# Kernel optimization log

Measured on AMD Instinct MI355X. Metric: run time of the kernel, lower is better.

The kernel has to match this reference:

```python
import jax, jax.numpy as jnp
import numpy as np

NH = 8          # attention heads
NC = 14         # disease classes
K = 10          # aspect queries per class
E = 1024        # vision_dim == text_dim
HID = 512       # hidden_dim = vision_dim // 2
TEMP = 0.1
LN_EPS = 1e-5


def _layernorm(x, g, b):
    m = jnp.mean(x, axis=-1, keepdims=True)
    v = jnp.mean(jnp.square(x - m), axis=-1, keepdims=True)
    return (x - m) * jax.lax.rsqrt(v + LN_EPS) * g + b


def _mha(q, k, v, in_w, in_b, out_w, out_b):
    # nn.MultiheadAttention (batch_first, eval mode => dropout off)
    B, Lq, Emb = q.shape
    Lk = k.shape[1]
    dh = Emb // NH
    wq, wk, wv = jnp.split(in_w, 3, axis=0)
    bq, bk, bv = jnp.split(in_b, 3)
    qh = (q @ wq.T + bq).reshape(B, Lq, NH, dh)
    kh = (k @ wk.T + bk).reshape(B, Lk, NH, dh)
    vh = (v @ wv.T + bv).reshape(B, Lk, NH, dh)
    scale = np.float32(1.0 / np.sqrt(dh))
    scores = jnp.einsum('bqhd,bkhd->bhqk', qh, kh) * scale
    attn = jax.nn.softmax(scores, axis=-1)
    out = jnp.einsum('bhqk,bkhd->bqhd', attn, vh).reshape(B, Lq, Emb)
    out = out @ out_w.T + out_b
    return out, attn.mean(axis=1)  # avg over heads, (B, Lq, Lk)


def _l2norm(x):
    return x / jnp.maximum(jnp.linalg.norm(x, axis=-1, keepdims=True), 1e-12)


def reference(vision_features, text_embeddings, vision_global, aspect_queries,
              ch_in_w, ch_in_b, ch_out_w, ch_out_b, tp_w, tp_b,
              ca_in_w, ca_in_b, ca_out_w, ca_out_b,
              cross_ln_g, cross_ln_b, cross_fc_w, cross_fc_b,
              dir_ln_g, dir_ln_b, dir_w1, dir_b1, dir_w2, dir_b2):
    B, N, _ = vision_features.shape
    # ---- contrastive branch (1-token query / 1-token kv attention) ----
    text_proj = text_embeddings @ tp_w.T + tp_b               # (B, E)
    c_out, _ = _mha(vision_global[:, None, :], text_proj[:, None, :],
                    text_proj[:, None, :], ch_in_w, ch_in_b, ch_out_w, ch_out_b)
    sim = jnp.sum(_l2norm(c_out[:, 0, :]) * _l2norm(text_proj), axis=-1) / TEMP  # (B,)
    contrastive_logits = jnp.broadcast_to(sim[:, None], (B, NC))
    # ---- supervised branch: fused per-class cross-attention (shared K/V) ----
    q = jnp.broadcast_to(aspect_queries.reshape(1, NC * K, E), (B, NC * K, E))
    att_out, attn_w = _mha(q, vision_features, vision_features,
                           ca_in_w, ca_in_b, ca_out_w, ca_out_b)
    attended = att_out.reshape(B, NC, K, E).mean(axis=2)       # (B, NC, E)
    attention_weights = attn_w.reshape(B, NC, K, N)            # (B, NC, K, N)
    # fc_cross: LN + per-class linear row (class j feature -> class j logit)
    h = _layernorm(attended, cross_ln_g, cross_ln_b)
    logits_cross = jnp.einsum('bjd,jd->bj', h, cross_fc_w) + cross_fc_b
    # fc_direct MLP on global feature
    g = _layernorm(vision_global, dir_ln_g, dir_ln_b)
    logits_direct = jax.nn.relu(g @ dir_w1.T + dir_b1) @ dir_w2.T + dir_b2
    supervised_logits = (logits_cross + logits_direct) * 0.5
    final_logits = (supervised_logits + contrastive_logits) * 0.5
    return contrastive_logits, supervised_logits, final_logits, attention_weights


def setup_inputs() -> dict:
    key = jax.random.key(0)
    ks = jax.random.split(key, 16)
    B, N = 64, 576
    w = lambda k, s: (jax.random.normal(k, s, dtype=jnp.float32) * 0.02)
    return {
        'vision_features': jax.random.normal(ks[0], (B, N, E), dtype=jnp.float32),
        'text_embeddings': jax.random.normal(ks[1], (B, E), dtype=jnp.float32),
        'vision_global': jax.random.normal(ks[2], (B, E), dtype=jnp.float32),
        'aspect_queries': jax.random.normal(ks[3], (NC, K, E), dtype=jnp.float32) / np.sqrt(E).astype(np.float32),
        'ch_in_w': w(ks[4], (3 * E, E)), 'ch_in_b': jnp.zeros((3 * E,), jnp.float32),
        'ch_out_w': w(ks[5], (E, E)), 'ch_out_b': jnp.zeros((E,), jnp.float32),
        'tp_w': w(ks[6], (E, E)), 'tp_b': jnp.zeros((E,), jnp.float32),
        'ca_in_w': w(ks[7], (3 * E, E)), 'ca_in_b': jnp.zeros((3 * E,), jnp.float32),
        'ca_out_w': w(ks[8], (E, E)), 'ca_out_b': jnp.zeros((E,), jnp.float32),
        'cross_ln_g': jnp.ones((E,), jnp.float32), 'cross_ln_b': jnp.zeros((E,), jnp.float32),
        'cross_fc_w': w(ks[9], (NC, E)), 'cross_fc_b': jnp.zeros((NC,), jnp.float32),
        'dir_ln_g': jnp.ones((E,), jnp.float32), 'dir_ln_b': jnp.zeros((E,), jnp.float32),
        'dir_w1': w(ks[10], (HID, E)), 'dir_b1': jnp.zeros((HID,), jnp.float32),
        'dir_w2': w(ks[11], (NC, HID)), 'dir_b2': jnp.zeros((NC,), jnp.float32),
    }
```

## Files before the change

kernel.cpp:

```cpp
#include <hip/hip_runtime.h>
#include <cstdio>
#include <cstdint>

using u16 = unsigned short;
typedef __bf16 bf16x8 __attribute__((ext_vector_type(8)));
typedef float f32x4 __attribute__((ext_vector_type(4)));

#define GLOBAL_AS __attribute__((address_space(1)))
#define LDS_AS __attribute__((address_space(3)))

__device__ __forceinline__ float bf2f(u16 h) {
  return __uint_as_float(((unsigned)h) << 16);
}
__device__ __forceinline__ u16 f2bf(float f) {
  unsigned u = __float_as_uint(f);
  u += 0x7FFFu + ((u >> 16) & 1u);
  return (u16)(u >> 16);
}

__device__ __forceinline__ void async_copy16(void* lds, const void* g) {
  __builtin_amdgcn_global_load_lds((const GLOBAL_AS unsigned int*)g,
                                   (LDS_AS unsigned int*)lds, 16, 0, 0);
}

__device__ __forceinline__ float block_sum(float v, float* red) {
#pragma unroll
  for (int o = 32; o >= 1; o >>= 1) v += __shfl_xor(v, o);
  __syncthreads();
  if ((threadIdx.x & 63) == 0) red[threadIdx.x >> 6] = v;
  __syncthreads();
  return red[0] + red[1] + red[2] + red[3];
}

__global__ __launch_bounds__(256) void cvt4_kernel(
    const float* __restrict__ s0, u16* __restrict__ d0,
    const float* __restrict__ s1, u16* __restrict__ d1,
    const float* __restrict__ s2, u16* __restrict__ d2,
    const float* __restrict__ s3, u16* __restrict__ d3) {
  const float* s; u16* d; long n; long b0; long nb;
  const int b = blockIdx.x;
  if (b < 2048)      { s = s0; d = d0; n = 37748736L; b0 = b;        nb = 2048; }
  else if (b < 2816) { s = s1; d = d1; n = 3145728L;  b0 = b - 2048; nb = 768; }
  else if (b < 3072) { s = s2; d = d2; n = 1048576L;  b0 = b - 2816; nb = 256; }
  else               { s = s3; d = d3; n = 143360L;   b0 = b - 3072; nb = 35; }
  long i = (b0 * 256 + threadIdx.x) * 4;
  const long stride = nb * 1024;
  for (; i < n; i += stride) {
    float4 v = *(const float4*)(s + i);
    ushort4 o;
    o.x = f2bf(v.x); o.y = f2bf(v.y); o.z = f2bf(v.z); o.w = f2bf(v.w);
    *(ushort4*)(d + i) = o;
  }
}

template <int VTD>
__global__ __launch_bounds__(512, 2) void gemm_kvq_kernel(
    const u16* __restrict__ A, const u16* __restrict__ Bkv,
    const u16* __restrict__ Aq, const u16* __restrict__ Bq,
    u16* __restrict__ Ck, u16* __restrict__ Cvp, u16* __restrict__ Vt,
    u16* __restrict__ Cq,
    const float* __restrict__ bias, const float* __restrict__ biasq) {
  __shared__ u16 lds[3][24576];
  const int bid = blockIdx.x;
  const int t = threadIdx.x;
  const int wid = t >> 6, l = t & 63;
  const int wr = wid >> 1, wc = wid & 1;
  const int lr = l & 15, lg = l >> 4, lr7 = lr & 7;

  int mt = 0, nt = 0, qb = -1;
  const u16* Abase; const u16* Bbase; const float* bias_b;
  if (bid < 2304) {
    const int wgid = (bid & 7) * 288 + (bid >> 3);
    mt = wgid >> 4; nt = wgid & 15;
    Abase = A + (size_t)mt * 256 * 1024;
    Bbase = Bkv + (size_t)nt * 128 * 1024;
    bias_b = bias + nt * 128;
  } else {
    qb = bid - 2304;
    Abase = Aq;
    Bbase = Bq + (size_t)qb * 128 * 1024;
    bias_b = biasq + qb * 128;
  }

  const int srow = t >> 3;
  const int scx = (t & 7) ^ (srow & 7);
  const char* Asrc = (const char*)Abase + (size_t)srow * 2048 + (scx << 4);
  const char* Bsrc = (const char*)Bbase + (size_t)srow * 2048 + (scx << 4);
  const int wbA = wid << 10;

  char* b0 = (char*)lds[0];
  char* b1 = (char*)lds[1];
  char* b2 = (char*)lds[2];

  f32x4 acc[4][4] = {};

#define STAGE3(dst, kt, part)                                               \
  {                                                                         \
    const size_t ko = (size_t)(kt) * 128;                                   \
    if ((part) == 0) {                                                      \
      async_copy16((dst) + wbA,          Asrc + ko);                        \
      async_copy16((dst) + 8192 + wbA,   Asrc + 131072 + ko);               \
      async_copy16((dst) + 16384 + wbA,  Asrc + 262144 + ko);               \
    } else {                                                                \
      async_copy16((dst) + 24576 + wbA,  Asrc + 393216 + ko);               \
      async_copy16((dst) + 32768 + wbA,  Bsrc + ko);                        \
      async_copy16((dst) + 40960 + wbA,  Bsrc + 131072 + ko);               \
    }                                                                       \
  }

#define COMPUTE_KS(p, KS)                                                   \
  {                                                                         \
    const int ccol = (((KS) << 2) | lg) ^ lr7;                              \
    const char* pA = (p) + (((wr << 6) + lr) << 7) + (ccol << 4);           \
    const char* pB = (p) + 32768 + (((wc << 6) + lr) << 7) + (ccol << 4);   \
    bf16x8 af[4], bfr[4];                                                   \
    _Pragma("unroll")                                                       \
    for (int i = 0; i < 4; ++i) {                                           \
      af[i]  = *(const bf16x8*)(pA + i * 2048);                             \
      bfr[i] = *(const bf16x8*)(pB + i * 2048);                             \
    }                                                                       \
    __builtin_amdgcn_s_setprio(1);                                          \
    _Pragma("unroll")                                                       \
    for (int mi = 0; mi < 4; ++mi)                                          \
      _Pragma("unroll")                                                     \
      for (int ni = 0; ni < 4; ++ni)                                        \
        acc[mi][ni] = __builtin_amdgcn_mfma_f32_16x16x32_bf16(              \
            af[mi], bfr[ni], acc[mi][ni], 0, 0, 0);                         \
    __builtin_amdgcn_s_setprio(0);                                          \
  }

  STAGE3(b0, 0, 0); STAGE3(b0, 0, 1);
  STAGE3(b1, 1, 0); STAGE3(b1, 1, 1);
  asm volatile("s_waitcnt vmcnt(6)" ::: "memory");
  __builtin_amdgcn_s_barrier();
  asm volatile("" ::: "memory");

  char* p0 = b0; char* p1 = b1; char* p2 = b2;
#pragma unroll 1
  for (int kt = 0; kt < 16; ++kt) {
    const bool pf = (kt < 14);
    if (pf) STAGE3(p2, kt + 2, 0);
    COMPUTE_KS(p0, 0);
    if (pf) STAGE3(p2, kt + 2, 1);
    COMPUTE_KS(p0, 1);
    if (kt < 15) {
      if (pf) asm volatile("s_waitcnt vmcnt(6)" ::: "memory");
      else    asm volatile("s_waitcnt vmcnt(0)" ::: "memory");
      __builtin_amdgcn_s_barrier();
      asm volatile("" ::: "memory");
    }
    char* tmp = p0; p0 = p1; p1 = p2; p2 = tmp;
  }
#undef STAGE3
#undef COMPUTE_KS

  const int mrow0 = wr * 64 + lg * 4;
  if (VTD && qb < 0 && nt >= 8) {
    __syncthreads();
    u16* T = (u16*)lds;
#pragma unroll
    for (int ni = 0; ni < 4; ++ni) {
      const int nl = wc * 64 + ni * 16 + lr;
      const float bv = bias_b[nl];
#pragma unroll
      for (int mi = 0; mi < 4; ++mi) {
        const int ml = mrow0 + mi * 16;
        ushort4 pk;
        pk.x = f2bf(acc[mi][ni][0] + bv);
        pk.y = f2bf(acc[mi][ni][1] + bv);
        pk.z = f2bf(acc[mi][ni][2] + bv);
        pk.w = f2bf(acc[mi][ni][3] + bv);
        *(ushort4*)(T + (size_t)nl * 264 + ml) = pk;
      }
    }
    __syncthreads();
    const int n_row = t >> 2, seg = t & 3;
    const int hh = nt - 8;
    const int m0 = mt * 256 + seg * 64;
    const int b = (unsigned)m0 / 576u;
    const int k0 = m0 - b * 576;
    u16* dst = Vt + ((size_t)(b * 8 + hh) * 128 + n_row) * 576 + k0;
    const u16* src = T + (size_t)n_row * 264 + seg * 64;
#pragma unroll
    for (int i = 0; i < 8; ++i)
      *(uint4*)(dst + i * 8) = *(const uint4*)(src + i * 8);
  } else {
    u16* Cb;
    if (qb >= 0)      Cb = Cq + (size_t)qb * 128;
    else if (nt < 8)  Cb = Ck + (size_t)nt * 128 + (size_t)mt * 256 * 1024;
    else              Cb = Cvp + (size_t)(nt - 8) * 128 + (size_t)mt * 256 * 1024;
#pragma unroll
    for (int ni = 0; ni < 4; ++ni) {
      const int nc = wc * 64 + ni * 16 + lr;
      const float bv = bias_b[nc];
#pragma unroll
      for (int mi = 0; mi < 4; ++mi) {
#pragma unroll
        for (int rg = 0; rg < 4; ++rg) {
          const size_t m = (size_t)(mrow0 + mi * 16 + rg);
          Cb[m * 1024 + nc] = f2bf(acc[mi][ni][rg] + bv);
        }
      }
    }
  }
}

template <int OUTF32>
__global__ __launch_bounds__(512, 2) void gemm_big_kernel(
    const u16* __restrict__ A, const u16* __restrict__ B, void* __restrict__ Cv,
    const float* __restrict__ bias, float scale,
    int KT, int ntx, int Mlim, int Nlim,
    long lda, long ldb, long ldc, int bdiv,
    long sA0, long sA1, long sB0, long sB1, long sC0, long sC1) {
  __shared__ u16 lds[3][24576];
  const int bid = blockIdx.x;
  const int bh = blockIdx.y;
  const int bb0 = bh / bdiv, bb1 = bh % bdiv;
  const int mt = bid / ntx, nt = bid % ntx;
  const int t = threadIdx.x;
  const int wid = t >> 6, l = t & 63;
  const int wr = wid >> 1, wc = wid & 1;
  const int lr = l & 15, lg = l >> 4, lr7 = lr & 7;

  const long ldab = lda * 2, ldbb = ldb * 2;
  const u16* Abase = A + (long)bb0 * sA0 + (long)bb1 * sA1 + (long)mt * 256 * lda;
  const u16* Bbase = B + (long)bb0 * sB0 + (long)bb1 * sB1 + (long)nt * 128 * ldb;

  const int srow = t >> 3;
  const int scx = (t & 7) ^ (srow & 7);
  const char* Asrc = (const char*)Abase + (long)srow * ldab + (scx << 4);
  const char* Bsrc = (const char*)Bbase + (long)srow * ldbb + (scx << 4);
  const int wbA = wid << 10;

  char* b0 = (char*)lds[0];
  char* b1 = (char*)lds[1];
  char* b2 = (char*)lds[2];

  f32x4 acc[4][4] = {};

#define STAGE3G(dst, kt, part)                                              \
  {                                                                         \
    const long ko = (long)(kt) * 128;                                       \
    if ((part) == 0) {                                                      \
      async_copy16((dst) + wbA,          Asrc + ko);                        \
      async_copy16((dst) + 8192 + wbA,   Asrc + 64 * ldab + ko);            \
      async_copy16((dst) + 16384 + wbA,  Asrc + 128 * ldab + ko);           \
    } else {                                                                \
      async_copy16((dst) + 24576 + wbA,  Asrc + 192 * ldab + ko);           \
      async_copy16((dst) + 32768 + wbA,  Bsrc + ko);                        \
      async_copy16((dst) + 40960 + wbA,  Bsrc + 64 * ldbb + ko);            \
    }                                                                       \
  }

#define COMPUTE_KS(p, KS)                                                   \
  {                                                                         \
    const int ccol = (((KS) << 2) | lg) ^ lr7;                              \
    const char* pA = (p) + (((wr << 6) + lr) << 7) + (ccol << 4);           \
    const char* pB = (p) + 32768 + (((wc << 6) + lr) << 7) + (ccol << 4);   \
    bf16x8 af[4], bfr[4];                                                   \
    _Pragma("unroll")                                                       \
    for (int i = 0; i < 4; ++i) {                                           \
      af[i]  = *(const bf16x8*)(pA + i * 2048);                             \
      bfr[i] = *(const bf16x8*)(pB + i * 2048);                             \
    }                                                                       \
    __builtin_amdgcn_s_setprio(1);                                          \
    _Pragma("unroll")                                                       \
    for (int mi = 0; mi < 4; ++mi)                                          \
      _Pragma("unroll")                                                     \
      for (int ni = 0; ni < 4; ++ni)                                        \
        acc[mi][ni] = __builtin_amdgcn_mfma_f32_16x16x32_bf16(              \
            af[mi], bfr[ni], acc[mi][ni], 0, 0, 0);                         \
    __builtin_amdgcn_s_setprio(0);                                          \
  }

  STAGE3G(b0, 0, 0); STAGE3G(b0, 0, 1);
  STAGE3G(b1, 1, 0); STAGE3G(b1, 1, 1);
  asm volatile("s_waitcnt vmcnt(6)" ::: "memory");
  __builtin_amdgcn_s_barrier();
  asm volatile("" ::: "memory");

  char* p0 = b0; char* p1 = b1; char* p2 = b2;
#pragma unroll 1
  for (int kt = 0; kt < KT; ++kt) {
    const bool pf = (kt < KT - 2);
    if (pf) STAGE3G(p2, kt + 2, 0);
    COMPUTE_KS(p0, 0);
    if (pf) STAGE3G(p2, kt + 2, 1);
    COMPUTE_KS(p0, 1);
    if (kt < KT - 1) {
      if (pf) asm volatile("s_waitcnt vmcnt(6)" ::: "memory");
      else    asm volatile("s_waitcnt vmcnt(0)" ::: "memory");
      __builtin_amdgcn_s_barrier();
      asm volatile("" ::: "memory");
    }
    char* tmp = p0; p0 = p1; p1 = p2; p2 = tmp;
  }
#undef STAGE3G
#undef COMPUTE_KS

  const long cBase = (long)bb0 * sC0 + (long)bb1 * sC1;
  const int mr0 = mt * 256 + wr * 64 + lg * 4;
  const int nc0 = nt * 128 + wc * 64 + lr;
#pragma unroll
  for (int ni = 0; ni < 4; ++ni) {
    const int n = nc0 + ni * 16;
    if (n >= Nlim) continue;
    const float bv = bias ? bias[n] : 0.0f;
#pragma unroll
    for (int mi = 0; mi < 4; ++mi) {
#pragma unroll
      for (int rg = 0; rg < 4; ++rg) {
        const int m = mr0 + mi * 16 + rg;
        if (m >= Mlim) continue;
        const float v = acc[mi][ni][rg] * scale + bv;
        if (OUTF32) ((float*)Cv)[cBase + (long)m * ldc + n] = v;
        else        ((u16*)Cv)[cBase + (long)m * ldc + n] = f2bf(v);
      }
    }
  }
}

__global__ __launch_bounds__(256) void transpose_v_kernel(const u16* __restrict__ V,
                                                          u16* __restrict__ Vt) {
  __shared__ u16 tile[64][65];
  const int k0 = blockIdx.x * 64;
  const int c0 = blockIdx.y * 64;
  const int b = blockIdx.z;
  const int t = threadIdx.x;
  const int tx = t & 15, ty = t >> 4;
  const u16* Vb = V + (size_t)(b * 576) * 1024;
#pragma unroll
  for (int i = 0; i < 4; ++i) {
    const int k = ty + i * 16;
    const u16* src = Vb + (size_t)(k0 + k) * 1024 + c0 + tx * 4;
    ushort2 v01 = *(const ushort2*)src;
    ushort2 v23 = *(const ushort2*)(src + 2);
    tile[k][tx * 4 + 0] = v01.x; tile[k][tx * 4 + 1] = v01.y;
    tile[k][tx * 4 + 2] = v23.x; tile[k][tx * 4 + 3] = v23.y;
  }
  __syncthreads();
  const int h = c0 >> 7, d0 = c0 & 127;
  u16* VtB = Vt + ((size_t)(b * 8 + h) * 128 + d0) * 576 + k0;
#pragma unroll
  for (int i = 0; i < 4; ++i) {
    const int d = ty + i * 16;
    u16* dst = VtB + (size_t)d * 576 + tx * 4;
    ushort2 a, bb2;
    a.x = tile[tx * 4 + 0][d]; a.y = tile[tx * 4 + 1][d];
    bb2.x = tile[tx * 4 + 2][d]; bb2.y = tile[tx * 4 + 3][d];
    *(ushort2*)dst = a; *(ushort2*)(dst + 2) = bb2;
  }
}

__global__ __launch_bounds__(512) void softmax_attn_kernel(u16* __restrict__ SP,
                                                           float* __restrict__ attnOut) {
  const int b = blockIdx.x, q = blockIdx.y;
  const int h = threadIdx.x >> 6, l = threadIdx.x & 63;
  __shared__ float pl[8][576];
  u16* row = SP + ((size_t)((b * 8 + h) * 144 + q)) * 576;
  float x[9];
#pragma unroll
  for (int i = 0; i < 9; ++i) x[i] = bf2f(row[l + 64 * i]);
  float m = x[0];
#pragma unroll
  for (int i = 1; i < 9; ++i) m = fmaxf(m, x[i]);
#pragma unroll
  for (int o = 32; o >= 1; o >>= 1) m = fmaxf(m, __shfl_xor(m, o));
  float e[9], s = 0.f;
#pragma unroll
  for (int i = 0; i < 9; ++i) { e[i] = expf(x[i] - m); s += e[i]; }
#pragma unroll
  for (int o = 32; o >= 1; o >>= 1) s += __shfl_xor(s, o);
  const float inv = 1.f / s;
#pragma unroll
  for (int i = 0; i < 9; ++i) {
    const float p = e[i] * inv;
    row[l + 64 * i] = f2bf(p);
    pl[h][l + 64 * i] = p;
  }
  __syncthreads();
  float* out = attnOut + ((size_t)(b * 140 + q)) * 576;
  for (int j = threadIdx.x; j < 576; j += 512) {
    float a = 0.f;
#pragma unroll
    for (int hh = 0; hh < 8; ++hh) a += pl[hh][j];
    out[j] = a * 0.125f;
  }
}

__global__ __launch_bounds__(256) void mean_o_kernel(const float* __restrict__ O,
                                                     u16* __restrict__ attended) {
  const int bc = blockIdx.x;
  const int b = bc / 14, c = bc % 14;
  const int t = threadIdx.x;
  const float* base = O + ((size_t)b * 140 + c * 10) * 1024;
#pragma unroll
  for (int i = 0; i < 4; ++i) {
    const int e = t + i * 256;
    float s = 0.f;
#pragma unroll
    for (int j = 0; j < 10; ++j) s += base[(size_t)j * 1024 + e];
    attended[(size_t)bc * 1024 + e] = f2bf(s * 0.1f);
  }
}

__global__ __launch_bounds__(256) void ln_crossfc_kernel(
    const float* __restrict__ ap, const float* __restrict__ g, const float* __restrict__ bb,
    const float* __restrict__ fw, const float* __restrict__ fb, float* __restrict__ out) {
  const int bc = blockIdx.x;
  const int c = bc % 14;
  const float* x = ap + (size_t)bc * 1024;
  __shared__ float red[4];
  const int t = threadIdx.x;
  float v[4];
  float s = 0.f;
#pragma unroll
  for (int i = 0; i < 4; ++i) { v[i] = x[t + i * 256]; s += v[i]; }
  const float mean = block_sum(s, red) * (1.f / 1024.f);
  float vs = 0.f;
#pragma unroll
  for (int i = 0; i < 4; ++i) { const float d = v[i] - mean; vs += d * d; }
  const float var = block_sum(vs, red) * (1.f / 1024.f);
  const float inv = rsqrtf(var + 1e-5f);
  float acc = 0.f;
#pragma unroll
  for (int i = 0; i < 4; ++i) {
    const int e = t + i * 256;
    const float h = (v[i] - mean) * inv * g[e] + bb[e];
    acc += h * fw[(size_t)c * 1024 + e];
  }
  acc = block_sum(acc, red);
  if (t == 0) out[bc] = acc + fb[c];
}

__global__ __launch_bounds__(256) void direct_mlp_kernel(
    const float* __restrict__ vg, const float* __restrict__ g, const float* __restrict__ bb,
    const float* __restrict__ w1, const float* __restrict__ b1,
    const float* __restrict__ w2, const float* __restrict__ b2, float* __restrict__ out) {
  const int b = blockIdx.x;
  __shared__ float red[4];
  __shared__ float gn[1024];
  __shared__ float h1[512];
  const int t = threadIdx.x;
  const float* x = vg + (size_t)b * 1024;
  float v[4];
  float s = 0.f;
#pragma unroll
  for (int i = 0; i < 4; ++i) { v[i] = x[t + i * 256]; s += v[i]; }
  const float mean = block_sum(s, red) * (1.f / 1024.f);
  float vs = 0.f;
#pragma unroll
  for (int i = 0; i < 4; ++i) { const float d = v[i] - mean; vs += d * d; }
  const float var = block_sum(vs, red) * (1.f / 1024.f);
  const float inv = rsqrtf(var + 1e-5f);
#pragma unroll
  for (int i = 0; i < 4; ++i) {
    const int e = t + i * 256;
    gn[e] = (v[i] - mean) * inv * g[e] + bb[e];
  }
  __syncthreads();
  for (int j = t; j < 512; j += 256) {
    float a = b1[j];
    const float4* wr = (const float4*)(w1 + (size_t)j * 1024);
    const float4* g4 = (const float4*)gn;
    for (int e = 0; e < 256; ++e) {
      float4 wv = wr[e], av = g4[e];
      a += av.x * wv.x + av.y * wv.y + av.z * wv.z + av.w * wv.w;
    }
    h1[j] = fmaxf(a, 0.f);
  }
  __syncthreads();
  for (int c = 0; c < 14; ++c) {
    float a = 0.f;
    for (int j = t; j < 512; j += 256) a += h1[j] * w2[(size_t)c * 512 + j];
    a = block_sum(a, red);
    if (t == 0) out[b * 14 + c] = a + b2[c];
  }
}

__global__ __launch_bounds__(256) void linear_f32_kernel(
    const float* __restrict__ A, const float* __restrict__ W, const float* __restrict__ bias,
    float* __restrict__ C, int N, int Kd) {
  const int r = blockIdx.x;
  const int j = blockIdx.y * 256 + threadIdx.x;
  __shared__ float a[1024];
  for (int e = threadIdx.x; e < Kd; e += 256) a[e] = A[(size_t)r * Kd + e];
  __syncthreads();
  float acc = bias ? bias[j] : 0.f;
  const float4* wr = (const float4*)(W + (size_t)j * Kd);
  const float4* a4 = (const float4*)a;
  for (int e = 0; e < Kd / 4; ++e) {
    float4 wv = wr[e], av = a4[e];
    acc += av.x * wv.x + av.y * wv.y + av.z * wv.z + av.w * wv.w;
  }
  C[(size_t)r * N + j] = acc;
}

__global__ __launch_bounds__(256) void sim_kernel(const float* __restrict__ co,
                                                  const float* __restrict__ tp,
                                                  float* __restrict__ sim) {
  const int b = blockIdx.x;
  const int t = threadIdx.x;
  __shared__ float red[4];
  const float* c = co + (size_t)b * 1024;
  const float* p = tp + (size_t)b * 1024;
  float dd = 0.f, nc = 0.f, nt = 0.f;
  for (int e = t; e < 1024; e += 256) {
    const float cv = c[e], pv = p[e];
    dd += cv * pv; nc += cv * cv; nt += pv * pv;
  }
  dd = block_sum(dd, red);
  nc = block_sum(nc, red);
  nt = block_sum(nt, red);
  if (t == 0)
    sim[b] = dd / (fmaxf(sqrtf(nc), 1e-12f) * fmaxf(sqrtf(nt), 1e-12f)) / 0.1f;
}

__global__ __launch_bounds__(256) void combine_kernel(const float* __restrict__ sim,
                                                      const float* __restrict__ lc,
                                                      const float* __restrict__ ld,
                                                      float* __restrict__ out) {
  const int i = blockIdx.x * 256 + threadIdx.x;
  if (i >= 896) return;
  const int b = i / 14;
  const float contr = sim[b];
  const float sup = 0.5f * (lc[i] + ld[i]);
  const float fin = 0.5f * (sup + contr);
  out[i] = contr;
  out[896 + i] = sup;
  out[1792 + i] = fin;
}

static constexpr size_t OFF_X    = 0;
static constexpr size_t OFF_K    = OFF_X + 75497472;
static constexpr size_t OFF_SP   = OFF_K + 75759616;
static constexpr size_t OFF_WIN  = OFF_SP + 85082112;
static constexpr size_t OFF_WOUT = OFF_WIN + 6291456;
static constexpr size_t OFF_ASP  = OFF_WOUT + 2097152;
static constexpr size_t OFF_QASP = OFF_ASP + 524288;
static constexpr size_t OFF_ATT  = OFF_QASP + 524288;
static constexpr size_t OFF_APRJ = OFF_ATT + 1835008;
static constexpr size_t OFF_TP   = OFF_APRJ + 3670016;
static constexpr size_t OFF_CV   = OFF_TP + 262144;
static constexpr size_t OFF_CO   = OFF_CV + 262144;
static constexpr size_t OFF_SIM  = OFF_CO + 262144;
static constexpr size_t OFF_LC   = OFF_SIM + 4096;
static constexpr size_t OFF_LD   = OFF_LC + 4096;
static constexpr size_t WS_SMALL = OFF_LD + 4096;
static constexpr size_t OFF_VT   = WS_SMALL;
static constexpr size_t WS_BIG   = OFF_VT + 75497472;

extern "C" void kernel_launch(void* const* d_in, const int* in_sizes, int n_in,
                              void* d_out, int out_size, void* d_ws, size_t ws_size,
                              hipStream_t stream) {
  (void)in_sizes; (void)n_in; (void)out_size;
  const float* vision_features = (const float*)d_in[0];
  const float* text_embeddings = (const float*)d_in[1];
  const float* vision_global   = (const float*)d_in[2];
  const float* aspect_queries  = (const float*)d_in[3];
  const float* ch_in_w  = (const float*)d_in[4];
  const float* ch_in_b  = (const float*)d_in[5];
  const float* ch_out_w = (const float*)d_in[6];
  const float* ch_out_b = (const float*)d_in[7];
  const float* tp_w = (const float*)d_in[8];
  const float* tp_b = (const float*)d_in[9];
  const float* ca_in_w  = (const float*)d_in[10];
  const float* ca_in_b  = (const float*)d_in[11];
  const float* ca_out_w = (const float*)d_in[12];
  const float* ca_out_b = (const float*)d_in[13];
  const float* cross_ln_g = (const float*)d_in[14];
  const float* cross_ln_b = (const float*)d_in[15];
  const float* cross_fc_w = (const float*)d_in[16];
  const float* cross_fc_b = (const float*)d_in[17];
  const float* dir_ln_g = (const float*)d_in[18];
  const float* dir_ln_b = (const float*)d_in[19];
  const float* dir_w1 = (const float*)d_in[20];
  const float* dir_b1 = (const float*)d_in[21];
  const float* dir_w2 = (const float*)d_in[22];
  const float* dir_b2 = (const float*)d_in[23];

  if (ws_size < WS_SMALL) {
    fprintf(stderr, "kernel_launch: ws too small: %zu < %zu\n", ws_size, WS_SMALL);
    return;
  }
  const bool big = (ws_size >= WS_BIG);

  char* ws = (char*)d_ws;
  u16* Xb      = (u16*)(ws + OFF_X);
  u16* Kb      = (u16*)(ws + OFF_K);
  float* O_all = (float*)(ws + OFF_K);
  u16* Vb      = (u16*)(ws + OFF_SP);
  u16* SP      = (u16*)(ws + OFF_SP);
  u16* Vt      = big ? (u16*)(ws + OFF_VT) : (u16*)(ws + OFF_X);
  u16* Win     = (u16*)(ws + OFF_WIN);
  u16* Wout    = (u16*)(ws + OFF_WOUT);
  u16* Asp     = (u16*)(ws + OFF_ASP);
  u16* Qasp    = (u16*)(ws + OFF_QASP);
  u16* Attd    = (u16*)(ws + OFF_ATT);
  float* Aprj  = (float*)(ws + OFF_APRJ);
  float* Tp    = (float*)(ws + OFF_TP);
  float* Cv2   = (float*)(ws + OFF_CV);
  float* Co    = (float*)(ws + OFF_CO);
  float* Sim   = (float*)(ws + OFF_SIM);
  float* Lc    = (float*)(ws + OFF_LC);
  float* Ld    = (float*)(ws + OFF_LD);
  float* attnOut = (float*)d_out + 2688;

  cvt4_kernel<<<3107, 256, 0, stream>>>(vision_features, Xb, ca_in_w, Win,
                                        ca_out_w, Wout, aspect_queries, Asp);

  if (big) {
    gemm_kvq_kernel<1><<<dim3(2312), 512, 0, stream>>>(
        Xb, Win + 1024 * 1024, Asp, Win, Kb, nullptr, Vt, Qasp,
        ca_in_b + 1024, ca_in_b);
  } else {
    gemm_kvq_kernel<0><<<dim3(2312), 512, 0, stream>>>(
        Xb, Win + 1024 * 1024, Asp, Win, Kb, Vb, nullptr, Qasp,
        ca_in_b + 1024, ca_in_b);
    transpose_v_kernel<<<dim3(9, 16, 64), 256, 0, stream>>>(Vb, Vt);
  }

  gemm_big_kernel<0><<<dim3(5, 512), 512, 0, stream>>>(
      Qasp, Kb, SP, nullptr, 0.08838834764831845f,
      2, 5, 140, 576, 1024, 1024, 576, 8,
      0L, 128L, 589824L, 128L, 663552L, 82944L);

  softmax_attn_kernel<<<dim3(64, 140), 512, 0, stream>>>(SP, attnOut);

  gemm_big_kernel<1><<<dim3(1, 512), 512, 0, stream>>>(
      SP, Vt, O_all, nullptr, 1.0f,
      9, 1, 140, 128, 576, 576, 1024, 8,
      663552L, 82944L, 589824L, 73728L, 143360L, 128L);

  mean_o_kernel<<<896, 256, 0, stream>>>(O_all, Attd);

  gemm_big_kernel<1><<<dim3(32, 1), 512, 0, stream>>>(
      Attd, Wout, Aprj, ca_out_b, 1.0f,
      16, 8, 896, 1024, 1024, 1024, 1024, 1,
      0L, 0L, 0L, 0L, 0L, 0L);

  ln_crossfc_kernel<<<896, 256, 0, stream>>>(Aprj, cross_ln_g, cross_ln_b,
                                             cross_fc_w, cross_fc_b, Lc);

  direct_mlp_kernel<<<64, 256, 0, stream>>>(vision_global, dir_ln_g, dir_ln_b,
                                            dir_w1, dir_b1, dir_w2, dir_b2, Ld);

  linear_f32_kernel<<<dim3(64, 4), 256, 0, stream>>>(text_embeddings, tp_w, tp_b, Tp, 1024, 1024);
  linear_f32_kernel<<<dim3(64, 4), 256, 0, stream>>>(Tp, ch_in_w + 2048 * 1024, ch_in_b + 2048, Cv2, 1024, 1024);
  linear_f32_kernel<<<dim3(64, 4), 256, 0, stream>>>(Cv2, ch_out_w, ch_out_b, Co, 1024, 1024);
  sim_kernel<<<64, 256, 0, stream>>>(Co, Tp, Sim);

  combine_kernel<<<4, 256, 0, stream>>>(Sim, Lc, Ld, (float*)d_out);
}
```

Measured before the change: 646.4 us.

## Enlarge KV/Q projection GEMM tile to 256x256 with double-buffered quarter pipeline

The fused K/V/Q projection GEMM moves from 256x128 tiles with a triple-buffered LDS ring to 256x256 tiles using 128KB of LDS, double buffering, and a 2x4 wave layout. Each wave now computes 128x64 with 32 accumulators. Loads of the next k-tile are split into quarter chunks and interleaved between four MFMA phases, with extra barriers in between. Larger tiles halve the block count and cut redundant global/L2 traffic for A and B. The cost is occupancy likely dropping to one block per CU, more barriers per iteration, and a V-transpose epilogue split into two passes.

```diff
diff --git a/kernel.cpp b/kernel.cpp
--- a/kernel.cpp
+++ b/kernel.cpp
@@ -60,145 +60,167 @@
     u16* __restrict__ Ck, u16* __restrict__ Cvp, u16* __restrict__ Vt,
     u16* __restrict__ Cq,
     const float* __restrict__ bias, const float* __restrict__ biasq) {
-  __shared__ u16 lds[3][24576];
+  __shared__ char smem[131072];
   const int bid = blockIdx.x;
   const int t = threadIdx.x;
   const int wid = t >> 6, l = t & 63;
-  const int wr = wid >> 1, wc = wid & 1;
+  const int wm = wid >> 2, wn = wid & 3;
   const int lr = l & 15, lg = l >> 4, lr7 = lr & 7;
 
   int mt = 0, nt = 0, qb = -1;
   const u16* Abase; const u16* Bbase; const float* bias_b;
-  if (bid < 2304) {
-    const int wgid = (bid & 7) * 288 + (bid >> 3);
-    mt = wgid >> 4; nt = wgid & 15;
+  if (bid < 1152) {
+    const int wgid = (bid & 7) * 144 + (bid >> 3);
+    mt = wgid >> 3; nt = wgid & 7;
     Abase = A + (size_t)mt * 256 * 1024;
-    Bbase = Bkv + (size_t)nt * 128 * 1024;
-    bias_b = bias + nt * 128;
+    Bbase = Bkv + (size_t)nt * 256 * 1024;
+    bias_b = bias + nt * 256;
   } else {
-    qb = bid - 2304;
+    qb = bid - 1152;
     Abase = Aq;
-    Bbase = Bq + (size_t)qb * 128 * 1024;
-    bias_b = biasq + qb * 128;
+    Bbase = Bq + (size_t)qb * 256 * 1024;
+    bias_b = biasq + qb * 256;
   }
 
   const int srow = t >> 3;
   const int scx = (t & 7) ^ (srow & 7);
   const char* Asrc = (const char*)Abase + (size_t)srow * 2048 + (scx << 4);
   const char* Bsrc = (const char*)Bbase + (size_t)srow * 2048 + (scx << 4);
-  const int wbA = wid << 10;
-
-  char* b0 = (char*)lds[0];
-  char* b1 = (char*)lds[1];
-  char* b2 = (char*)lds[2];
-
-  f32x4 acc[4][4] = {};
-
-#define STAGE3(dst, kt, part)                                               \
-  {                                                                         \
-    const size_t ko = (size_t)(kt) * 128;                                   \
-    if ((part) == 0) {                                                      \
-      async_copy16((dst) + wbA,          Asrc + ko);                        \
-      async_copy16((dst) + 8192 + wbA,   Asrc + 131072 + ko);               \
-      async_copy16((dst) + 16384 + wbA,  Asrc + 262144 + ko);               \
-    } else {                                                                \
-      async_copy16((dst) + 24576 + wbA,  Asrc + 393216 + ko);               \
-      async_copy16((dst) + 32768 + wbA,  Bsrc + ko);                        \
-      async_copy16((dst) + 40960 + wbA,  Bsrc + 131072 + ko);               \
-    }                                                                       \
-  }
-
-#define COMPUTE_KS(p, KS)                                                   \
-  {                                                                         \
-    const int ccol = (((KS) << 2) | lg) ^ lr7;                              \
-    const char* pA = (p) + (((wr << 6) + lr) << 7) + (ccol << 4);           \
-    const char* pB = (p) + 32768 + (((wc << 6) + lr) << 7) + (ccol << 4);   \
-    bf16x8 af[4], bfr[4];                                                   \
-    _Pragma("unroll")                                                       \
-    for (int i = 0; i < 4; ++i) {                                           \
-      af[i]  = *(const bf16x8*)(pA + i * 2048);                             \
-      bfr[i] = *(const bf16x8*)(pB + i * 2048);                             \
-    }                                                                       \
-    __builtin_amdgcn_s_setprio(1);                                          \
-    _Pragma("unroll")                                                       \
-    for (int mi = 0; mi < 4; ++mi)                                          \
-      _Pragma("unroll")                                                     \
-      for (int ni = 0; ni < 4; ++ni)                                        \
-        acc[mi][ni] = __builtin_amdgcn_mfma_f32_16x16x32_bf16(              \
-            af[mi], bfr[ni], acc[mi][ni], 0, 0, 0);                         \
-    __builtin_amdgcn_s_setprio(0);                                          \
-  }
-
-  STAGE3(b0, 0, 0); STAGE3(b0, 0, 1);
-  STAGE3(b1, 1, 0); STAGE3(b1, 1, 1);
-  asm volatile("s_waitcnt vmcnt(6)" ::: "memory");
+  const int wb = wid << 10;
+
+  f32x4 acc[8][4] = {};
+
+#define SA(d, r, kt) async_copy16(smem + (d)*65536 + (r)*8192 + wb, \
+                                  Asrc + (size_t)(r)*131072 + (size_t)(kt)*128)
+#define SB(d, r, kt) async_copy16(smem + (d)*65536 + 32768 + (r)*8192 + wb, \
+                                  Bsrc + (size_t)(r)*131072 + (size_t)(kt)*128)
+
+#define RA(d, half)                                                          \
+  _Pragma("unroll")                                                          \
+  for (int i = 0; i < 4; ++i) {                                              \
+    const int row = wm * 128 + ((half)*4 + i) * 16 + lr;                     \
+    af[i][0] = *(const bf16x8*)(smem + (d)*65536 + (row << 7) + ((lg ^ lr7) << 4));       \
+    af[i][1] = *(const bf16x8*)(smem + (d)*65536 + (row << 7) + (((4 | lg) ^ lr7) << 4)); \
+  }
+
+#define RB(d, half)                                                          \
+  _Pragma("unroll")                                                          \
+  for (int j = 0; j < 2; ++j) {                                              \
+    const int row = wn * 64 + ((half)*2 + j) * 16 + lr;                      \
+    bfr[j][0] = *(const bf16x8*)(smem + (d)*65536 + 32768 + (row << 7) + ((lg ^ lr7) << 4));       \
+    bfr[j][1] = *(const bf16x8*)(smem + (d)*65536 + 32768 + (row << 7) + (((4 | lg) ^ lr7) << 4)); \
+  }
+
+#define MM(mh, nh)                                                           \
+  __builtin_amdgcn_s_setprio(1);                                             \
+  _Pragma("unroll")                                                          \
+  for (int ks = 0; ks < 2; ++ks)                                             \
+    _Pragma("unroll")                                                        \
+    for (int i = 0; i < 4; ++i)                                              \
+      _Pragma("unroll")                                                      \
+      for (int j = 0; j < 2; ++j)                                            \
+        acc[(mh)*4 + i][(nh)*2 + j] = __builtin_amdgcn_mfma_f32_16x16x32_bf16( \
+            af[i][ks], bfr[j][ks], acc[(mh)*4 + i][(nh)*2 + j], 0, 0, 0);    \
+  __builtin_amdgcn_s_setprio(0);
+
+  SA(0, 0, 0); SA(0, 1, 0); SA(0, 2, 0); SA(0, 3, 0);
+  SB(0, 0, 0); SB(0, 1, 0); SB(0, 2, 0); SB(0, 3, 0);
+  SA(1, 0, 1); SA(1, 2, 1);
+  asm volatile("s_waitcnt vmcnt(2)" ::: "memory");
   __builtin_amdgcn_s_barrier();
   asm volatile("" ::: "memory");
 
-  char* p0 = b0; char* p1 = b1; char* p2 = b2;
 #pragma unroll 1
   for (int kt = 0; kt < 16; ++kt) {
-    const bool pf = (kt < 14);
-    if (pf) STAGE3(p2, kt + 2, 0);
-    COMPUTE_KS(p0, 0);
-    if (pf) STAGE3(p2, kt + 2, 1);
-    COMPUTE_KS(p0, 1);
-    if (kt < 15) {
-      if (pf) asm volatile("s_waitcnt vmcnt(6)" ::: "memory");
-      else    asm volatile("s_waitcnt vmcnt(0)" ::: "memory");
-      __builtin_amdgcn_s_barrier();
-      asm volatile("" ::: "memory");
+    const int cur = kt & 1, nxt = cur ^ 1;
+    const bool pf1 = (kt < 15), pf2 = (kt < 14);
+    bf16x8 af[4][2], bfr[2][2];
+    RA(cur, 0);
+    RB(cur, 0);
+    if (pf1) { SB(nxt, 0, kt + 1); SB(nxt, 1, kt + 1); }
+    __builtin_amdgcn_s_barrier();
+    asm volatile("s_waitcnt lgkmcnt(0)" ::: "memory");
+    MM(0, 0);
+    __builtin_amdgcn_s_barrier();
+    RB(cur, 1);
+    if (pf1) { SB(nxt, 2, kt + 1); SB(nxt, 3, kt + 1); }
+    __builtin_amdgcn_s_barrier();
+    asm volatile("s_waitcnt lgkmcnt(0)" ::: "memory");
+    MM(0, 1);
+    if (pf1) asm volatile("s_waitcnt vmcnt(6)" ::: "memory");
+    __builtin_amdgcn_s_barrier();
+    RA(cur, 1);
+    if (pf1) { SA(nxt, 1, kt + 1); SA(nxt, 3, kt + 1); }
+    __builtin_amdgcn_s_barrier();
+    asm volatile("s_waitcnt lgkmcnt(0)" ::: "memory");
+    MM(1, 1);
+    __builtin_amdgcn_s_barrier();
+    RB(cur, 0);
+    if (pf2) { SA(cur, 0, kt + 2); SA(cur, 2, kt + 2); }
+    __builtin_amdgcn_s_barrier();
+    asm volatile("s_waitcnt lgkmcnt(0)" ::: "memory");
+    MM(1, 0);
+    if (pf2)      asm volatile("s_waitcnt vmcnt(4)" ::: "memory");
+    else if (pf1) asm volatile("s_waitcnt vmcnt(0)" ::: "memory");
+    __builtin_amdgcn_s_barrier();
+  }
+#undef SA
+#undef SB
+#undef RA
+#undef RB
+#undef MM
+
+  if (VTD && qb < 0 && nt >= 4) {
+    u16* T = (u16*)smem;
+    const int vc2 = t >> 1, seg = t & 1;
+    const int vglob = (nt - 4) * 256 + vc2;
+    const int h2 = vglob >> 7, d2 = vglob & 127;
+#pragma unroll 1
+    for (int mh = 0; mh < 2; ++mh) {
+      __syncthreads();
+      if (wm == mh) {
+#pragma unroll
+        for (int ni = 0; ni < 4; ++ni) {
+          const int vc = wn * 64 + ni * 16 + lr;
+          const float bv = bias_b[vc];
+#pragma unroll
+          for (int mi = 0; mi < 8; ++mi) {
+            const int ml = mi * 16 + lg * 4;
+            ushort4 pk;
+            pk.x = f2bf(acc[mi][ni][0] + bv);
+            pk.y = f2bf(acc[mi][ni][1] + bv);
+            pk.z = f2bf(acc[mi][ni][2] + bv);
+            pk.w = f2bf(acc[mi][ni][3] + bv);
+            *(ushort4*)(T + (size_t)vc * 136 + ml) = pk;
+          }
+        }
+      }
+      __syncthreads();
+      const int mg0 = mt * 256 + mh * 128 + seg * 64;
+      const int bb = (unsigned)mg0 / 576u;
+      const int k0 = mg0 - bb * 576;
+      u16* dst = Vt + ((size_t)(bb * 8 + h2) * 128 + d2) * 576 + k0;
+      const u16* src = T + (size_t)vc2 * 136 + seg * 64;
+#pragma unroll
+      for (int i2 = 0; i2 < 8; ++i2)
+        *(uint4*)(dst + i2 * 8) = *(const uint4*)(src + i2 * 8);
     }
-    char* tmp = p0; p0 = p1; p1 = p2; p2 = tmp;
-  }
-#undef STAGE3
-#undef COMPUTE_KS
-
-  const int mrow0 = wr * 64 + lg * 4;
-  if (VTD && qb < 0 && nt >= 8) {
-    __syncthreads();
-    u16* T = (u16*)lds;
+  } else {
+    u16* D; int cb0;
+    if (qb >= 0)      { D = Cq;  cb0 = qb * 256; }
+    else if (nt < 4)  { D = Ck;  cb0 = nt * 256; }
+    else              { D = Cvp; cb0 = (nt - 4) * 256; }
 #pragma unroll
     for (int ni = 0; ni < 4; ++ni) {
-      const int nl = wc * 64 + ni * 16 + lr;
-      const float bv = bias_b[nl];
-#pragma unroll
-      for (int mi = 0; mi < 4; ++mi) {
-        const int ml = mrow0 + mi * 16;
-        ushort4 pk;
-        pk.x = f2bf(acc[mi][ni][0] + bv);
-        pk.y = f2bf(acc[mi][ni][1] + bv);
-        pk.z = f2bf(acc[mi][ni][2] + bv);
-        pk.w = f2bf(acc[mi][ni][3] + bv);
-        *(ushort4*)(T + (size_t)nl * 264 + ml) = pk;
-      }
-    }
-    __syncthreads();
-    const int n_row = t >> 2, seg = t & 3;
-    const int hh = nt - 8;
-    const int m0 = mt * 256 + seg * 64;
-    const int b = (unsigned)m0 / 576u;
-    const int k0 = m0 - b * 576;
-    u16* dst = Vt + ((size_t)(b * 8 + hh) * 128 + n_row) * 576 + k0;
-    const u16* src = T + (size_t)n_row * 264 + seg * 64;
-#pragma unroll
-    for (int i = 0; i < 8; ++i)
-      *(uint4*)(dst + i * 8) = *(const uint4*)(src + i * 8);
-  } else {
-    u16* Cb;
-    if (qb >= 0)      Cb = Cq + (size_t)qb * 128;
-    else if (nt < 8)  Cb = Ck + (size_t)nt * 128 + (size_t)mt * 256 * 1024;
-    else              Cb = Cvp + (size_t)(nt - 8) * 128 + (size_t)mt * 256 * 1024;
-#pragma unroll
-    for (int ni = 0; ni < 4; ++ni) {
-      const int nc = wc * 64 + ni * 16 + lr;
+      const int nc = wn * 64 + ni * 16 + lr;
       const float bv = bias_b[nc];
-#pragma unroll
-      for (int mi = 0; mi < 4; ++mi) {
+      const int col = cb0 + nc;
+#pragma unroll
+      for (int mi = 0; mi < 8; ++mi) {
 #pragma unroll
         for (int rg = 0; rg < 4; ++rg) {
-          const size_t m = (size_t)(mrow0 + mi * 16 + rg);
-          Cb[m * 1024 + nc] = f2bf(acc[mi][ni][rg] + bv);
+          const size_t m = (size_t)mt * 256 + wm * 128 + mi * 16 + lg * 4 + rg;
+          D[m * 1024 + col] = f2bf(acc[mi][ni][rg] + bv);
         }
       }
     }
@@ -610,11 +632,11 @@
                                         ca_out_w, Wout, aspect_queries, Asp);
 
   if (big) {
-    gemm_kvq_kernel<1><<<dim3(2312), 512, 0, stream>>>(
+    gemm_kvq_kernel<1><<<dim3(1156), 512, 0, stream>>>(
         Xb, Win + 1024 * 1024, Asp, Win, Kb, nullptr, Vt, Qasp,
         ca_in_b + 1024, ca_in_b);
   } else {
-    gemm_kvq_kernel<0><<<dim3(2312), 512, 0, stream>>>(
+    gemm_kvq_kernel<0><<<dim3(1156), 512, 0, stream>>>(
         Xb, Win + 1024 * 1024, Asp, Win, Kb, Vb, nullptr, Qasp,
         ca_in_b + 1024, ca_in_b);
     transpose_v_kernel<<<dim3(9, 16, 64), 256, 0, stream>>>(Vb, Vt);
```

Result: no change. 637.2 us (-1.4%).
